# Kernel optimization log

Hardware: AMD Instinct MI355X
Metric: run time of the kernel (lower is better)

Reference implementation:

```python
import jax, jax.numpy as jnp
import numpy as np

N1, N2, F = 2048, 32768, 64
SPATIAL = 512  # fine (big) spatial size
I = 3          # 2**I * coarse_size = SPATIAL


def setup_inputs() -> dict:
    key = jax.random.key(0)
    k1, k2, k3 = jax.random.split(key, 3)
    coarse_size = SPATIAL // (2 ** I)  # 64
    # coarse voxel coords: 3 spatial dims in [0, coarse_size), batch col = 0
    fm_sp = jax.random.randint(k1, (N1, 3), 0, coarse_size)
    feature_map = jnp.concatenate([fm_sp, jnp.zeros((N1, 1), jnp.int32)], axis=1).astype(jnp.float32)
    # fine voxel coords: 3 spatial dims in [0, SPATIAL), batch col = 0
    co_sp = jax.random.randint(k2, (N2, 3), 0, SPATIAL)
    coords = jnp.concatenate([co_sp, jnp.zeros((N2, 1), jnp.int32)], axis=1).astype(jnp.float32)
    x_features = jax.random.normal(k3, (N1, F), dtype=jnp.float32)
    return {"feature_map": feature_map, "x_features": x_features, "coords": coords, "i": I}


def reference(feature_map, x_features, coords, i):
    scale = 2 ** i
    # (N1,1,4) vs (1,N2,4) broadcast containment test (all 4 columns, incl. batch id,
    # are scaled — faithful to the original module)
    fm_scaled = feature_map * scale                      # (N1,4)
    lo = fm_scaled[:, None, :] <= coords[None, :, :]     # (N1,N2,4)
    hi = (fm_scaled[:, None, :] + scale) > coords[None, :, :]
    index = lo.all(-1) & hi.all(-1)                      # (N1,N2) bool
    # torch.t(index).argmax(dim=1): for each fine voxel, first coarse voxel containing it
    sel = jnp.argmax(index, axis=0)                      # (N2,)
    final_features = x_features[sel]                     # (N2,F)
    final_coords = feature_map[sel]                      # (N2,4)
    return final_coords, final_features
```

## Files before the change

kernel.cpp:

```cpp
#include <hip/hip_runtime.h>

#define N1 2048
#define N2 32768
#define F  64
#define SPATIAL 512


__global__ void efm_populate(const float* __restrict__ fm,
                             const int* __restrict__ ip,
                             unsigned* __restrict__ grid) {
    int n1 = blockIdx.x * blockDim.x + threadIdx.x;
    if (n1 >= N1) return;
    int i  = ip[0];
    int cs = SPATIAL >> i;
    float4 f = ((const float4*)fm)[n1];
    int x = (int)f.x, y = (int)f.y, z = (int)f.z;
    atomicMin(&grid[(x * cs + y) * cs + z], (unsigned)n1);
}

__global__ void efm_gather(const float* __restrict__ fm,
                           const float* __restrict__ xf,
                           const float* __restrict__ co,
                           const int*   __restrict__ ip,
                           const unsigned* __restrict__ grid,
                           float* __restrict__ out_coords,
                           float* __restrict__ out_feats) {
    int tid = blockIdx.x * blockDim.x + threadIdx.x;
    int n2  = tid >> 4;
    int sub = tid & 15;
    if (n2 >= N2) return;
    int i  = ip[0];
    int cs = SPATIAL >> i;
    float4 c = ((const float4*)co)[n2];
    int cx = ((int)c.x) >> i;
    int cy = ((int)c.y) >> i;
    int cz = ((int)c.z) >> i;
    unsigned sel = grid[(cx * cs + cy) * cs + cz];
    if (sel >= (unsigned)N1) sel = 0;
    ((float4*)out_feats)[n2 * (F / 4) + sub] =
        ((const float4*)xf)[sel * (F / 4) + sub];
    if (sub == 0)
        ((float4*)out_coords)[n2] = ((const float4*)fm)[sel];
}

__global__ void efm_brute(const float* __restrict__ fm,
                          const float* __restrict__ xf,
                          const float* __restrict__ co,
                          const int*   __restrict__ ip,
                          float* __restrict__ out_coords,
                          float* __restrict__ out_feats) {
    int tid  = blockIdx.x * blockDim.x + threadIdx.x;
    int n2   = tid >> 6;
    int lane = tid & 63;
    if (n2 >= N2) return;
    float scale = (float)(1 << ip[0]);
    float4 c = ((const float4*)co)[n2];
    int sel = 0;
    for (int base = 0; base < N1; base += 64) {
        float4 f = ((const float4*)fm)[base + lane];
        bool m = (f.x * scale <= c.x) && (f.x * scale + scale > c.x)
              && (f.y * scale <= c.y) && (f.y * scale + scale > c.y)
              && (f.z * scale <= c.z) && (f.z * scale + scale > c.z)
              && (f.w * scale <= c.w) && (f.w * scale + scale > c.w);
        unsigned long long b = __ballot(m);
        if (b) { sel = base + __ffsll((unsigned long long)b) - 1; break; }
    }
    out_feats[n2 * F + lane] = xf[sel * F + lane];
    if (lane < 4) out_coords[n2 * 4 + lane] = fm[sel * 4 + lane];
}

extern "C" void kernel_launch(void* const* d_in, const int* in_sizes, int n_in,
                              void* d_out, int out_size, void* d_ws, size_t ws_size,
                              hipStream_t stream) {
    const float* fm = (const float*)d_in[0];
    const float* xf = (const float*)d_in[1];
    const float* co = (const float*)d_in[2];
    const int*   ip = (const int*)d_in[3];

    float* out_coords = (float*)d_out;
    float* out_feats  = (float*)d_out + N2 * 4;

    const size_t grid_cells = 64 * 64 * 64;
    if (ws_size >= grid_cells * sizeof(unsigned)) {
        unsigned* grid = (unsigned*)d_ws;
        efm_populate<<<(N1 + 255) / 256, 256, 0, stream>>>(fm, ip, grid);
        efm_gather<<<(N2 * 16 + 255) / 256, 256, 0, stream>>>(
            fm, xf, co, ip, grid, out_coords, out_feats);
    } else {
        efm_brute<<<(N2 * 64 + 255) / 256, 256, 0, stream>>>(
            fm, xf, co, ip, out_coords, out_feats);
    }
}
```

Baseline: 65.50 us.

## Fuse coarse-voxel lookup into one kernel using a shared-memory occupancy bitmap

The global-workspace grid (populate plus gather) and the brute-force fallback are replaced by a single kernel. Each block builds a shared-memory bitmap of occupied coarse cells plus a cell-index array from all coarse voxels. For each fine voxel, the bitmap is tested first. Only on a hit does the wave do a ballot-based linear scan to find the lowest matching coarse index; the feature rows are then gathered with float4 stores. This removes the workspace dependency and the second launch. The cost is that every block redundantly reads all coarse voxels and zeroes 32KB of LDS, which also limits occupancy.

```diff
diff --git a/kernel.cpp b/kernel.cpp
--- a/kernel.cpp
+++ b/kernel.cpp
@@ -5,68 +5,76 @@
 #define F  64
 #define SPATIAL 512
 
+__global__ __launch_bounds__(256) void efm_onepass(
+        const float* __restrict__ fm,
+        const float* __restrict__ xf,
+        const float* __restrict__ co,
+        const int*   __restrict__ ip,
+        float* __restrict__ out_coords,
+        float* __restrict__ out_feats) {
+    __shared__ __align__(16) unsigned bitmap[8192];
+    __shared__ int cells[N1];
 
-__global__ void efm_populate(const float* __restrict__ fm,
-                             const int* __restrict__ ip,
-                             unsigned* __restrict__ grid) {
-    int n1 = blockIdx.x * blockDim.x + threadIdx.x;
-    if (n1 >= N1) return;
-    int i  = ip[0];
-    int cs = SPATIAL >> i;
-    float4 f = ((const float4*)fm)[n1];
-    int x = (int)f.x, y = (int)f.y, z = (int)f.z;
-    atomicMin(&grid[(x * cs + y) * cs + z], (unsigned)n1);
-}
+    const int t  = threadIdx.x;
+    const int i  = ip[0];
+    const int cs = SPATIAL >> i;
+    const bool bm_ok = (cs <= 64);
 
-__global__ void efm_gather(const float* __restrict__ fm,
-                           const float* __restrict__ xf,
-                           const float* __restrict__ co,
-                           const int*   __restrict__ ip,
-                           const unsigned* __restrict__ grid,
-                           float* __restrict__ out_coords,
-                           float* __restrict__ out_feats) {
-    int tid = blockIdx.x * blockDim.x + threadIdx.x;
-    int n2  = tid >> 4;
-    int sub = tid & 15;
-    if (n2 >= N2) return;
-    int i  = ip[0];
-    int cs = SPATIAL >> i;
-    float4 c = ((const float4*)co)[n2];
-    int cx = ((int)c.x) >> i;
-    int cy = ((int)c.y) >> i;
-    int cz = ((int)c.z) >> i;
-    unsigned sel = grid[(cx * cs + cy) * cs + cz];
-    if (sel >= (unsigned)N1) sel = 0;
-    ((float4*)out_feats)[n2 * (F / 4) + sub] =
-        ((const float4*)xf)[sel * (F / 4) + sub];
-    if (sub == 0)
-        ((float4*)out_coords)[n2] = ((const float4*)fm)[sel];
-}
+    uint4 z4 = make_uint4(0u, 0u, 0u, 0u);
+    #pragma unroll
+    for (int j = 0; j < 8; ++j)
+        ((uint4*)bitmap)[t + 256 * j] = z4;
+    int cellr[8];
+    #pragma unroll
+    for (int j = 0; j < 8; ++j) {
+        int n1 = t + 256 * j;
+        float4 f = ((const float4*)fm)[n1];
+        int cell = (((int)f.x) * cs + ((int)f.y)) * cs + ((int)f.z);
+        cellr[j] = cell;
+        cells[n1] = cell;
+    }
+    __syncthreads();
+    if (bm_ok) {
+        #pragma unroll
+        for (int j = 0; j < 8; ++j)
+            atomicOr(&bitmap[cellr[j] >> 5], 1u << (cellr[j] & 31));
+    }
+    __syncthreads();
 
-__global__ void efm_brute(const float* __restrict__ fm,
-                          const float* __restrict__ xf,
-                          const float* __restrict__ co,
-                          const int*   __restrict__ ip,
-                          float* __restrict__ out_coords,
-                          float* __restrict__ out_feats) {
-    int tid  = blockIdx.x * blockDim.x + threadIdx.x;
-    int n2   = tid >> 6;
-    int lane = tid & 63;
-    if (n2 >= N2) return;
-    float scale = (float)(1 << ip[0]);
-    float4 c = ((const float4*)co)[n2];
+    const int wv    = t >> 6;
+    const int lane  = t & 63;
+    const int vbase = blockIdx.x * 64 + wv * 16;
+    const int v16   = lane & 15;
+
+    float4 c = ((const float4*)co)[vbase + v16];
+    int cx = ((int)c.x) >> i, cy = ((int)c.y) >> i, cz = ((int)c.z) >> i;
+    int cell = (cx * cs + cy) * cs + cz;
+    bool hit = bm_ok ? (((bitmap[cell >> 5] >> (cell & 31)) & 1u) != 0u) : true;
     int sel = 0;
-    for (int base = 0; base < N1; base += 64) {
-        float4 f = ((const float4*)fm)[base + lane];
-        bool m = (f.x * scale <= c.x) && (f.x * scale + scale > c.x)
-              && (f.y * scale <= c.y) && (f.y * scale + scale > c.y)
-              && (f.z * scale <= c.z) && (f.z * scale + scale > c.z)
-              && (f.w * scale <= c.w) && (f.w * scale + scale > c.w);
-        unsigned long long b = __ballot(m);
-        if (b) { sel = base + __ffsll((unsigned long long)b) - 1; break; }
+    unsigned m16 = (unsigned)(__ballot(hit) & 0xFFFFull);
+    while (m16) {
+        int vv = __ffs(m16) - 1;
+        m16 &= m16 - 1;
+        int target = __shfl(cell, vv);
+        for (int base = 0; base < N1; base += 64) {
+            unsigned long long b = __ballot(cells[base + lane] == target);
+            if (b) {
+                int idx = base + __ffsll(b) - 1;
+                if (v16 == vv) sel = idx;
+                break;
+            }
+        }
     }
-    out_feats[n2 * F + lane] = xf[sel * F + lane];
-    if (lane < 4) out_coords[n2 * 4 + lane] = fm[sel * 4 + lane];
+
+    #pragma unroll
+    for (int r = 0; r < 4; ++r) {
+        int vv   = r * 4 + (lane >> 4);
+        int selv = __shfl(sel, vv);
+        ((float4*)out_feats)[(vbase + vv) * (F / 4) + v16] =
+            ((const float4*)xf)[selv * (F / 4) + v16];
+    }
+    if (lane < 16)
+        ((float4*)out_coords)[vbase + lane] = ((const float4*)fm)[sel];
 }
 
 extern "C" void kernel_launch(void* const* d_in, const int* in_sizes, int n_in,
@@ -80,14 +88,6 @@
     float* out_coords = (float*)d_out;
     float* out_feats  = (float*)d_out + N2 * 4;
 
-    const size_t grid_cells = 64 * 64 * 64;
-    if (ws_size >= grid_cells * sizeof(unsigned)) {
-        unsigned* grid = (unsigned*)d_ws;
-        efm_populate<<<(N1 + 255) / 256, 256, 0, stream>>>(fm, ip, grid);
-        efm_gather<<<(N2 * 16 + 255) / 256, 256, 0, stream>>>(
-            fm, xf, co, ip, grid, out_coords, out_feats);
-    } else {
-        efm_brute<<<(N2 * 64 + 255) / 256, 256, 0, stream>>>(
-            fm, xf, co, ip, out_coords, out_feats);
-    }
+    efm_onepass<<<N2 / 64, 256, 0, stream>>>(
+        fm, xf, co, ip, out_coords, out_feats);
 }
```

Measured after the change: 65.17 us. No clear change (-0.5%).
